# Kernel tuning notes

Measured on AMD Instinct MI355X. Metric: run time of the kernel, lower is better.

## Reference

```python
import jax, jax.numpy as jnp
import numpy as np

WS = 8          # window_size
OWS = 12        # overlap_win_size = int(8*0.5)+8
PAD = 2         # (OWS-WS)//2
HEADS = 6
DH = 16         # dim_head
INNER = HEADS * DH  # 96
SCALE = DH ** -0.5


def rel_to_abs(x):
    # x: (b, l, m) with m = 2*r - 1
    b, l, m = x.shape
    r = (m + 1) // 2
    x = jnp.concatenate([x, jnp.zeros((b, l, 1), x.dtype)], axis=2)
    flat = x.reshape(b, l * (m + 1))
    flat = jnp.concatenate([flat, jnp.zeros((b, m - l), x.dtype)], axis=1)
    final = flat.reshape(b, l + 1, m)[:, :l, m - r:]
    return final  # (b, l, r)


def relative_logits_1d(q, rel_k):
    # q: (B, X, Y, d), rel_k: (2r-1, d)
    B, X, Y, _ = q.shape
    r = (rel_k.shape[0] + 1) // 2
    logits = jnp.einsum('bxyd,rd->bxyr', q, rel_k)           # (B, X, Y, 2r-1)
    logits = rel_to_abs(logits.reshape(B * X, Y, -1)).reshape(B, X, Y, r)
    logits = jnp.broadcast_to(logits[:, :, None], (B, X, r, Y, r))  # b x i y j
    return logits


def rel_pos_emb(q, rel_height, rel_width):
    # q: (B, WS*WS, d) -> bias (B, WS*WS, OWS*OWS)
    B, _, d = q.shape
    qg = q.reshape(B, WS, WS, d)
    lw = relative_logits_1d(qg, rel_width)                   # (B, x, i, y, j)
    lw = lw.transpose(0, 1, 3, 2, 4).reshape(B, WS * WS, OWS * OWS)  # b (x y) (i j)
    lh = relative_logits_1d(qg.transpose(0, 2, 1, 3), rel_height)    # (B, y, i, x, j) roles swapped
    lh = lh.transpose(0, 3, 1, 4, 2).reshape(B, WS * WS, OWS * OWS)  # b (y x) (j i)
    return lw + lh


def unfold_windows(t, nh, nw):
    # torch nn.Unfold(kernel=OWS, stride=WS, padding=PAD) then
    # rearrange 'b (c j) i -> (b i) j c' -> (b*nh*nw, OWS*OWS, C)
    b, C, _, _ = t.shape
    tp = jnp.pad(t, ((0, 0), (0, 0), (PAD, PAD), (PAD, PAD)))
    ridx = (jnp.arange(nh) * WS)[:, None] + jnp.arange(OWS)   # (nh, OWS)
    cidx = (jnp.arange(nw) * WS)[:, None] + jnp.arange(OWS)   # (nw, OWS)
    p = tp[:, :, ridx, :]            # (b, C, nh, OWS, Wp)
    p = p[:, :, :, :, cidx]          # (b, C, nh, OWS, nw, OWS)
    p = p.transpose(0, 2, 4, 3, 5, 1)  # (b, nh, nw, OWS, OWS, C)
    return p.reshape(b * nh * nw, OWS * OWS, C)


def split_heads(t):
    # (B, n, heads*dh) -> (B*heads, n, dh)
    B, n, _ = t.shape
    return t.reshape(B, n, HEADS, DH).transpose(0, 2, 1, 3).reshape(B * HEADS, n, DH)


def setup_inputs() -> dict:
    key = jax.random.key(0)
    k = jax.random.split(key, 5)
    x = jax.random.normal(k[0], (2, 96, 256, 256), jnp.float32)
    qkv_w = jax.random.normal(k[1], (288, 96), jnp.float32) * 0.05
    qkv_b = jnp.zeros((288,), jnp.float32)
    proj_w = jax.random.normal(k[2], (96, 96), jnp.float32) * 0.05
    proj_b = jnp.zeros((96,), jnp.float32)
    rel_height = jax.random.normal(k[3], (23, 16), jnp.float32) * SCALE
    rel_width = jax.random.normal(k[4], (23, 16), jnp.float32) * SCALE
    return {"x": x, "qkv_w": qkv_w, "qkv_b": qkv_b, "proj_w": proj_w,
            "proj_b": proj_b, "rel_height": rel_height, "rel_width": rel_width}


def reference(x, qkv_w, qkv_b, proj_w, proj_b, rel_height, rel_width):
    b, c, h, w = x.shape
    nh, nw = h // WS, w // WS
    qkv = jnp.einsum('oc,bchw->bohw', qkv_w, x) + qkv_b[None, :, None, None]
    qs, ks, vs = jnp.split(qkv, 3, axis=1)  # each (b, INNER, h, w)
    # queries: non-overlapping windows 'b c (h p1) (w p2) -> (b h w) (p1 p2) c'
    qs = qs.reshape(b, INNER, nh, WS, nw, WS).transpose(0, 2, 4, 3, 5, 1)
    qs = qs.reshape(b * nh * nw, WS * WS, INNER)
    ks = unfold_windows(ks, nh, nw)  # (b*nh*nw, OWS*OWS, INNER)
    vs = unfold_windows(vs, nh, nw)
    qs, ks, vs = map(split_heads, (qs, ks, vs))  # (B*heads, n, DH)
    qs = qs * SCALE
    attn = jnp.einsum('bqd,bkd->bqk', qs, ks)
    attn = attn + rel_pos_emb(qs, rel_height, rel_width)
    attn = jax.nn.softmax(attn, axis=-1)
    out = jnp.einsum('bqk,bkd->bqd', attn, vs)  # (b*nh*nw*heads, WS*WS, DH)
    out = out.reshape(b, nh, nw, HEADS, WS, WS, DH)
    out = out.transpose(0, 3, 6, 1, 4, 2, 5).reshape(b, INNER, h, w)
    out = jnp.einsum('oc,bchw->bohw', proj_w, out) + proj_b[None, :, None, None]
    return out
```

## Files before the change

### kernel.cpp

```cpp
#include <hip/hip_runtime.h>
#include <hip/hip_bf16.h>


typedef __attribute__((ext_vector_type(8))) short bf16x8;
typedef __attribute__((ext_vector_type(4))) float f32x4;

__device__ __forceinline__ f32x4 mfma16(bf16x8 a, bf16x8 b, f32x4 c) {
  return __builtin_amdgcn_mfma_f32_16x16x32_bf16(a, b, c, 0, 0, 0);
}
__device__ __forceinline__ short f2b(float f) {
  unsigned u = __builtin_bit_cast(unsigned, f);
  unsigned r = u + 0x7fffu + ((u >> 16) & 1u);
  return (short)(r >> 16);
}
__device__ __forceinline__ unsigned cvtpk(float lo, float hi) {
  unsigned r;
  asm("v_cvt_pk_bf16_f32 %0, %1, %2" : "=v"(r) : "v"(lo), "v"(hi));
  return r;
}
__device__ __forceinline__ void splitf(float x, short& h, short& l) {
  unsigned u = __builtin_bit_cast(unsigned, x);
  h = (short)(u >> 16);
  float fh = __builtin_bit_cast(float, u & 0xffff0000u);
  l = f2b(x - fh);
}

#define KPLANE 1081600L

__global__ __launch_bounds__(256) void prep_kernel(
    const float* __restrict__ qkv_w, const float* __restrict__ proj_w,
    const float* __restrict__ rel_h, const float* __restrict__ rel_w,
    short* __restrict__ qwh, short* __restrict__ qwl,
    short* __restrict__ pwh, short* __restrict__ pwl,
    short* __restrict__ rhb, short* __restrict__ rwb,
    short* __restrict__ k_t) {
  int i = blockIdx.x * 256 + threadIdx.x;
  if (i < 288 * 96) {
    short h, l;
    splitf(qkv_w[i], h, l);
    qwh[i] = h;
    qwl[i] = l;
  }
  if (i < 96 * 96) {
    short h, l;
    splitf(proj_w[i], h, l);
    pwh[i] = h;
    pwl[i] = l;
  }
  if (i < 368) {
    rhb[i] = f2b(rel_h[i]);
    rwb[i] = f2b(rel_w[i]);
  }
  if (i < 12 * 2064) {
    int plane = i / 2064, r = i - plane * 2064;
    int py, px;
    if (r < 1040) {
      int rowid = r / 260;
      py = (rowid < 2) ? rowid : 256 + rowid;
      px = r - rowid * 260;
    } else {
      int r2 = r - 1040;
      py = 2 + (r2 >> 2);
      int cid = r2 & 3;
      px = (cid < 2) ? cid : 256 + cid;
    }
    bf16x8 z = {0, 0, 0, 0, 0, 0, 0, 0};
    long base = (long)plane * KPLANE + (long)(py * 260 + px) * 16;
    *(bf16x8*)(k_t + base) = z;
    *(bf16x8*)(k_t + base + 8) = z;
  }
}

__global__ __launch_bounds__(256) void qkv_kernel(
    const float* __restrict__ x, const short* __restrict__ qwh,
    const short* __restrict__ qwl, const float* __restrict__ bias,
    short* __restrict__ q_t, short* __restrict__ k_t,
    short* __restrict__ v_t) {
  __shared__ __attribute__((aligned(16))) short Ah[4][32][104];
  const int tid = threadIdx.x;
  const int wave = tid >> 6, lane = tid & 63;
  const int quad = lane >> 4, col = lane & 15;
  const long P0 = (long)blockIdx.x * 128 + wave * 32;
  const int b = (int)(P0 >> 16);
  const int hw0 = (int)(P0 & 65535);

  {
    const long base = ((long)b * 96) << 16;
    const int px0 = (lane & 7) * 4;
    for (int i = 0; i < 12; ++i) {
      int c = i * 8 + (lane >> 3);
      float4 v = *(const float4*)(x + base + ((long)c << 16) + hw0 + px0);
      Ah[wave][px0][c] = f2b(v.x);
      Ah[wave][px0 + 1][c] = f2b(v.y);
      Ah[wave][px0 + 2][c] = f2b(v.z);
      Ah[wave][px0 + 3][c] = f2b(v.w);
    }
  }
  bf16x8 af[2][3];
  for (int mt = 0; mt < 2; ++mt)
    for (int ks = 0; ks < 3; ++ks)
      af[mt][ks] = *(const bf16x8*)&Ah[wave][mt * 16 + col][ks * 32 + quad * 8];

  for (int t = 0; t < 3; ++t) {
    const float scale = (t == 0) ? 0.25f * 1.44269504f : 1.0f;
    for (int i6 = 0; i6 < 6; ++i6) {
      const int o = (t * 6 + i6) * 16 + col;
      bf16x8 bh[3], bl[3];
      for (int ks = 0; ks < 3; ++ks) {
        bh[ks] = *(const bf16x8*)(qwh + o * 96 + ks * 32 + quad * 8);
        bl[ks] = *(const bf16x8*)(qwl + o * 96 + ks * 32 + quad * 8);
      }
      float bv = bias[o];
      f32x4 acc0 = {bv, bv, bv, bv}, acc1 = acc0;
      for (int ks = 0; ks < 3; ++ks) {
        acc0 = mfma16(af[0][ks], bh[ks], acc0);
        acc0 = mfma16(af[0][ks], bl[ks], acc0);
        acc1 = mfma16(af[1][ks], bh[ks], acc1);
        acc1 = mfma16(af[1][ks], bl[ks], acc1);
      }
      for (int r = 0; r < 4; ++r) {
        Ah[wave][quad * 4 + r][i6 * 16 + col] = f2b(acc0[r] * scale);
        Ah[wave][16 + quad * 4 + r][i6 * 16 + col] = f2b(acc1[r] * scale);
      }
    }
    if (t == 1) {
      const int py = (hw0 >> 8) + 2;
      const int pxb = (hw0 & 255) + 2;
      for (int i = 0; i < 6; ++i) {
        int linear = i * 64 + lane;
        int px = linear / 12, c = linear - px * 12;
        int h = c >> 1, half = c & 1;
        bf16x8 vv = *(const bf16x8*)&Ah[wave][px][c * 8];
        *(bf16x8*)(k_t + (long)(h * 2 + b) * KPLANE +
                   (long)(py * 260 + pxb + px) * 16 + half * 8) = vv;
      }
    } else {
      short* plane0 = (t == 0) ? q_t : v_t;
      for (int i = 0; i < 6; ++i) {
        int linear = i * 64 + lane;
        int px = linear / 12, c = linear - px * 12;
        int h = c >> 1, half = c & 1;
        bf16x8 vv = *(const bf16x8*)&Ah[wave][px][c * 8];
        *(bf16x8*)(plane0 + (long)h * 2097152 + (P0 + px) * 16 + half * 8) =
            vv;
      }
    }
  }
}

__global__ __launch_bounds__(256) void attn_kernel(
    const short* __restrict__ q_t, const short* __restrict__ k_t,
    const short* __restrict__ v_t, const short* __restrict__ rhb,
    const short* __restrict__ rwb, short* __restrict__ ao) {
  __shared__ __attribute__((aligned(16))) short v_lds[16][168];
  __shared__ __attribute__((aligned(16))) char scratch[4][5248];

  const int orig = blockIdx.x, head = blockIdx.y;
  const int win = ((orig & 7) << 8) | (orig >> 3);
  const int b = win >> 10, wy = (win & 1023) >> 5, wx = win & 31;
  const int y0 = wy * 8 - 2, x0 = wx * 8 - 2;
  const long pb = (long)b << 16;
  const int tid = threadIdx.x;

  if (tid < 160) {
    const int key = tid;
    bool valid = false;
    long pix = 0;
    if (key < 144) {
      int kh = key / 12, kw = key - kh * 12;
      int gy = y0 + kh, gx = x0 + kw;
      valid = ((unsigned)gy < 256u) && ((unsigned)gx < 256u);
      pix = pb + gy * 256 + gx;
    }
    if (valid) {
      const short* src = v_t + (long)head * 2097152 + pix * 16;
      union { bf16x8 v; short s[8]; } u0, u1;
      u0.v = *(const bf16x8*)src;
      u1.v = *(const bf16x8*)(src + 8);
      for (int d = 0; d < 8; ++d) {
        v_lds[d][key] = u0.s[d];
        v_lds[d + 8][key] = u1.s[d];
      }
    } else {
      for (int d = 0; d < 16; ++d) v_lds[d][key] = 0;
    }
  }
  __syncthreads();

  const int wave = tid >> 6, lane = tid & 63;
  const int quad = lane >> 4, col = lane & 15;
  float* dWs = (float*)scratch[wave];
  float* dHt = dWs + 600;
  unsigned* ppd = (unsigned*)scratch[wave];

  const short* qp = q_t + (long)head * 2097152;
  const short* kpb = k_t + (long)(head * 2 + b) * KPLANE;

  bf16x8 qf = {0, 0, 0, 0, 0, 0, 0, 0};
  if (quad < 2) {
    int qg = wave * 16 + col;
    int qy = qg >> 3, qx = qg & 7;
    qf = *(const bf16x8*)(qp + (pb + (wy * 8 + qy) * 256 + wx * 8 + qx) * 16 +
                          quad * 8);
  }

  for (int nt = 0; nt < 2; ++nt) {
    int r = nt * 16 + col;
    bf16x8 bw = {0, 0, 0, 0, 0, 0, 0, 0}, bh2 = bw;
    if (quad < 2 && r < 23) {
      bw = *(const bf16x8*)(rwb + r * 16 + quad * 8);
      bh2 = *(const bf16x8*)(rhb + r * 16 + quad * 8);
    }
    f32x4 z = {0.f, 0.f, 0.f, 0.f};
    f32x4 aw = mfma16(qf, bw, z);
    f32x4 ah = mfma16(qf, bh2, z);
    if (r < 23)
      for (int r4 = 0; r4 < 4; ++r4) {
        int ql = quad * 4 + r4;
        dWs[(r + (ql & 7)) * 20 + ql] = aw[r4];
        dHt[r * 20 + ql] = ah[r4];
      }
  }

  f32x4 L[9];
  {
    int kh = (col >= 12) ? 1 : 0, kw = col - 12 * kh;
    const short* ka =
        kpb + (long)((wy * 8 + kh) * 260 + wx * 8 + kw) * 16 + quad * 8;
    for (int nt = 0; nt < 9; ++nt) {
      bf16x8 kf = *(const bf16x8*)ka;
      f32x4 z = {0.f, 0.f, 0.f, 0.f};
      L[nt] = mfma16(qf, kf, z);
      kw += 4;
      if (kw >= 12) {
        kw -= 12;
        ka += 512 * 16;
      } else {
        ka += 264 * 16;
      }
    }
  }

  const int qy4 = wave * 2 + (quad >> 1);
  {
    int kh = (col >= 12) ? 1 : 0, kw = col - 12 * kh;
    for (int nt = 0; nt < 9; ++nt) {
      f32x4 wv = *(const f32x4*)&dWs[(11 + kw) * 20 + quad * 4];
      f32x4 hv = *(const f32x4*)&dHt[(11 + kh - qy4) * 20 + quad * 4];
      for (int r4 = 0; r4 < 4; ++r4)
        L[nt][r4] = __builtin_amdgcn_exp2f(L[nt][r4] + wv[r4] + hv[r4]);
      kw += 4;
      kh += 1;
      if (kw >= 12) {
        kw -= 12;
        kh += 1;
      }
    }
  }
  asm volatile("" ::: "memory");

  for (int nt = 0; nt < 9; ++nt) {
    unsigned d0 = cvtpk(L[nt][0], L[nt][1]);
    unsigned d1 = cvtpk(L[nt][2], L[nt][3]);
    int base = (nt * 16 + col) * 9 + quad * 2;
    ppd[base] = d0;
    ppd[base + 1] = d1;
  }

  const unsigned sel = (col & 1) ? 0x07060302u : 0x05040100u;
  const bf16x8 ones = {0x3F80, 0x3F80, 0x3F80, 0x3F80,
                       0x3F80, 0x3F80, 0x3F80, 0x3F80};
  f32x4 oacc = {0.f, 0.f, 0.f, 0.f}, oaccS = oacc;
  for (int ks = 0; ks < 5; ++ks) {
    int k0 = ks * 32 + quad * 8;
    bool live = k0 < 144;
    int k0c = live ? k0 : 136;
    const unsigned* rp = ppd + k0c * 9 + (col >> 1);
    unsigned r0 = rp[0], r1 = rp[9], r2 = rp[18], r3 = rp[27];
    unsigned r4v = rp[36], r5 = rp[45], r6 = rp[54], r7 = rp[63];
    union { unsigned u[4]; bf16x8 v; } pu;
    pu.u[0] = live ? __builtin_amdgcn_perm(r1, r0, sel) : 0u;
    pu.u[1] = live ? __builtin_amdgcn_perm(r3, r2, sel) : 0u;
    pu.u[2] = live ? __builtin_amdgcn_perm(r5, r4v, sel) : 0u;
    pu.u[3] = live ? __builtin_amdgcn_perm(r7, r6, sel) : 0u;
    bf16x8 vb = *(const bf16x8*)&v_lds[col][ks * 32 + quad * 8];
    oacc = mfma16(pu.v, vb, oacc);
    oaccS = mfma16(pu.v, ones, oaccS);
  }
  for (int r4 = 0; r4 < 4; ++r4) {
    int qg = wave * 16 + quad * 4 + r4;
    int qy = qg >> 3, qx = qg & 7;
    float val = oacc[r4] * __builtin_amdgcn_rcpf(oaccS[r4]);
    ao[(long)head * 2097152 +
       (pb + (wy * 8 + qy) * 256 + wx * 8 + qx) * 16 + col] = f2b(val);
  }
}

__global__ __launch_bounds__(256) void proj_kernel(
    const short* __restrict__ ao, const short* __restrict__ pwh,
    const short* __restrict__ pwl, const float* __restrict__ bias,
    float* __restrict__ out) {
  const int tid = threadIdx.x;
  const int wave = tid >> 6, lane = tid & 63;
  const int quad = lane >> 4, col = lane & 15;
  const long P0 = (long)blockIdx.x * 128 + wave * 32;

  bf16x8 bfr[2][3];
  for (int nt = 0; nt < 2; ++nt) {
    long pix = P0 + nt * 16 + col;
    for (int ks = 0; ks < 3; ++ks) {
      int c0 = ks * 32 + quad * 8;
      bfr[nt][ks] = *(const bf16x8*)(ao + (long)(c0 >> 4) * 2097152 +
                                     pix * 16 + (c0 & 15));
    }
  }
  f32x4 acc[6][2];
  for (int mt = 0; mt < 6; ++mt) {
    for (int r = 0; r < 4; ++r) {
      float bv = bias[mt * 16 + quad * 4 + r];
      acc[mt][0][r] = bv;
      acc[mt][1][r] = bv;
    }
    bf16x8 afh[3], afl[3];
    for (int ks = 0; ks < 3; ++ks) {
      afh[ks] =
          *(const bf16x8*)(pwh + (mt * 16 + col) * 96 + ks * 32 + quad * 8);
      afl[ks] =
          *(const bf16x8*)(pwl + (mt * 16 + col) * 96 + ks * 32 + quad * 8);
    }
    for (int ks = 0; ks < 3; ++ks) {
      acc[mt][0] = mfma16(afh[ks], bfr[0][ks], acc[mt][0]);
      acc[mt][0] = mfma16(afl[ks], bfr[0][ks], acc[mt][0]);
      acc[mt][1] = mfma16(afh[ks], bfr[1][ks], acc[mt][1]);
      acc[mt][1] = mfma16(afl[ks], bfr[1][ks], acc[mt][1]);
    }
  }
  const int bb = (int)(P0 >> 16);
  const int hw0 = (int)(P0 & 65535);
  for (int mt = 0; mt < 6; ++mt)
    for (int nt = 0; nt < 2; ++nt)
      for (int r = 0; r < 4; ++r) {
        int o = mt * 16 + quad * 4 + r;
        int hw = hw0 + nt * 16 + col;
        out[(((long)(bb * 96 + o)) << 16) + hw] = acc[mt][nt][r];
      }
}

extern "C" void kernel_launch(void* const* d_in, const int* in_sizes, int n_in,
                              void* d_out, int out_size, void* d_ws,
                              size_t ws_size, hipStream_t stream) {
  const float* x = (const float*)d_in[0];
  const float* qkv_w = (const float*)d_in[1];
  const float* qkv_b = (const float*)d_in[2];
  const float* proj_w = (const float*)d_in[3];
  const float* proj_b = (const float*)d_in[4];
  const float* rel_h = (const float*)d_in[5];
  const float* rel_w = (const float*)d_in[6];

  const long NPIXC = 131072L * 96L;
  short* q_t = (short*)d_ws;
  short* k_t = q_t + NPIXC;
  short* v_t = k_t + 12 * KPLANE;
  short* ao = v_t + NPIXC;
  short* qwh = ao + NPIXC;
  short* qwl = qwh + 288 * 96;
  short* pwh = qwl + 288 * 96;
  short* pwl = pwh + 96 * 96;
  short* rhb = pwl + 96 * 96;
  short* rwb = rhb + 368;
  float* out = (float*)d_out;

  hipLaunchKernelGGL(prep_kernel, dim3(108), dim3(256), 0, stream, qkv_w,
                     proj_w, rel_h, rel_w, qwh, qwl, pwh, pwl, rhb, rwb, k_t);
  hipLaunchKernelGGL(qkv_kernel, dim3(1024), dim3(256), 0, stream, x, qwh, qwl,
                     qkv_b, q_t, k_t, v_t);
  hipLaunchKernelGGL(attn_kernel, dim3(2048, 6), dim3(256), 0, stream, q_t,
                     k_t, v_t, rhb, rwb, ao);
  hipLaunchKernelGGL(proj_kernel, dim3(1024), dim3(256), 0, stream, ao, pwh,
                     pwl, proj_b, out);
}
```

Measured before the change: 200.2 us.

## Transpose qkv and proj GEMMs so weights are the A operand and drop LDS staging

The QKV kernel now puts the weight tile in the MFMA A operand and the pixel tile in B. Input pixels load straight from global memory into registers as bf16, with no shared-memory transpose, and each wave covers 64 pixels instead of 32. The query scale is folded into the prepared weights and a precomputed scaled bias. Output columns are written as packed 32-bit stores, and the next weight slice is prefetched while the current one computes. The projection kernel gets the same restructuring, writing fp32 output in coalesced per-channel rows. The cost is more registers per thread and half as many blocks.

```diff
diff --git a/kernel.cpp b/kernel.cpp
--- a/kernel.cpp
+++ b/kernel.cpp
@@ -26,18 +26,22 @@
 }
 
 #define KPLANE 1081600L
+#define QS (0.25f * 1.44269504f)
 
 __global__ __launch_bounds__(256) void prep_kernel(
     const float* __restrict__ qkv_w, const float* __restrict__ proj_w,
     const float* __restrict__ rel_h, const float* __restrict__ rel_w,
+    const float* __restrict__ qkv_b,
     short* __restrict__ qwh, short* __restrict__ qwl,
     short* __restrict__ pwh, short* __restrict__ pwl,
     short* __restrict__ rhb, short* __restrict__ rwb,
-    short* __restrict__ k_t) {
+    float* __restrict__ sbias, short* __restrict__ k_t) {
   int i = blockIdx.x * 256 + threadIdx.x;
   if (i < 288 * 96) {
+    float wv = qkv_w[i];
+    if (i < 96 * 96) wv *= QS;
     short h, l;
-    splitf(qkv_w[i], h, l);
+    splitf(wv, h, l);
     qwh[i] = h;
     qwl[i] = l;
   }
@@ -51,6 +55,7 @@
     rhb[i] = f2b(rel_h[i]);
     rwb[i] = f2b(rel_w[i]);
   }
+  if (i < 288) sbias[i] = qkv_b[i] * (i < 96 ? QS : 1.0f);
   if (i < 12 * 2064) {
     int plane = i / 2064, r = i - plane * 2064;
     int py, px;
@@ -73,76 +78,92 @@
 
 __global__ __launch_bounds__(256) void qkv_kernel(
     const float* __restrict__ x, const short* __restrict__ qwh,
-    const short* __restrict__ qwl, const float* __restrict__ bias,
+    const short* __restrict__ qwl, const float* __restrict__ sbias,
     short* __restrict__ q_t, short* __restrict__ k_t,
     short* __restrict__ v_t) {
-  __shared__ __attribute__((aligned(16))) short Ah[4][32][104];
   const int tid = threadIdx.x;
   const int wave = tid >> 6, lane = tid & 63;
   const int quad = lane >> 4, col = lane & 15;
-  const long P0 = (long)blockIdx.x * 128 + wave * 32;
-  const int b = (int)(P0 >> 16);
-  const int hw0 = (int)(P0 & 65535);
-
-  {
-    const long base = ((long)b * 96) << 16;
-    const int px0 = (lane & 7) * 4;
-    for (int i = 0; i < 12; ++i) {
-      int c = i * 8 + (lane >> 3);
-      float4 v = *(const float4*)(x + base + ((long)c << 16) + hw0 + px0);
-      Ah[wave][px0][c] = f2b(v.x);
-      Ah[wave][px0 + 1][c] = f2b(v.y);
-      Ah[wave][px0 + 2][c] = f2b(v.z);
-      Ah[wave][px0 + 3][c] = f2b(v.w);
-    }
-  }
-  bf16x8 af[2][3];
-  for (int mt = 0; mt < 2; ++mt)
+  const int blk = blockIdx.x;
+  const int b = blk >> 8, row = blk & 255;
+
+  const float* xw = x + (((long)b * 96) << 16) + row * 256 + wave * 64 + col;
+  bf16x8 bx[4][3];
+#pragma unroll
+  for (int tile = 0; tile < 4; ++tile)
+#pragma unroll
+    for (int ks = 0; ks < 3; ++ks) {
+      const float* p = xw + tile * 16 + (((long)(ks * 32 + quad * 8)) << 16);
+      float v0 = p[0];
+      float v1 = p[1L << 16];
+      float v2 = p[2L << 16];
+      float v3 = p[3L << 16];
+      float v4 = p[4L << 16];
+      float v5 = p[5L << 16];
+      float v6 = p[6L << 16];
+      float v7 = p[7L << 16];
+      union { unsigned u[4]; bf16x8 w; } t;
+      t.u[0] = cvtpk(v0, v1);
+      t.u[1] = cvtpk(v2, v3);
+      t.u[2] = cvtpk(v4, v5);
+      t.u[3] = cvtpk(v6, v7);
+      bx[tile][ks] = t.w;
+    }
+
+  const short* wbh = qwh + col * 96 + quad * 8;
+  const short* wbl = qwl + col * 96 + quad * 8;
+  bf16x8 wh[3], wl[3];
+#pragma unroll
+  for (int ks = 0; ks < 3; ++ks) {
+    wh[ks] = *(const bf16x8*)(wbh + ks * 32);
+    wl[ks] = *(const bf16x8*)(wbl + ks * 32);
+  }
+
+  const long pixb = (long)blk * 256 + wave * 64 + col;
+  short* kbase = k_t + (long)b * KPLANE +
+                 ((long)((row + 2) * 260 + wave * 64 + col + 2)) * 16 +
+                 quad * 4;
+
+#pragma unroll
+  for (int t6 = 0; t6 < 18; ++t6) {
+    bf16x8 nh[3], nl[3];
+    if (t6 < 17) {
+#pragma unroll
+      for (int ks = 0; ks < 3; ++ks) {
+        nh[ks] = *(const bf16x8*)(wbh + (t6 + 1) * 1536 + ks * 32);
+        nl[ks] = *(const bf16x8*)(wbl + (t6 + 1) * 1536 + ks * 32);
+      }
+    }
+    f32x4 bv = *(const f32x4*)(sbias + t6 * 16 + quad * 4);
+    f32x4 acc[4] = {bv, bv, bv, bv};
+#pragma unroll
     for (int ks = 0; ks < 3; ++ks)
-      af[mt][ks] = *(const bf16x8*)&Ah[wave][mt * 16 + col][ks * 32 + quad * 8];
-
-  for (int t = 0; t < 3; ++t) {
-    const float scale = (t == 0) ? 0.25f * 1.44269504f : 1.0f;
-    for (int i6 = 0; i6 < 6; ++i6) {
-      const int o = (t * 6 + i6) * 16 + col;
-      bf16x8 bh[3], bl[3];
+#pragma unroll
+      for (int tile = 0; tile < 4; ++tile) {
+        acc[tile] = mfma16(wh[ks], bx[tile][ks], acc[tile]);
+        acc[tile] = mfma16(wl[ks], bx[tile][ks], acc[tile]);
+      }
+#pragma unroll
+    for (int tile = 0; tile < 4; ++tile) {
+      unsigned d0 = cvtpk(acc[tile][0], acc[tile][1]);
+      unsigned d1 = cvtpk(acc[tile][2], acc[tile][3]);
+      if (t6 >= 6 && t6 < 12) {
+        short* kp = kbase + (long)(t6 - 6) * (2 * KPLANE) + tile * 256;
+        *(unsigned*)kp = d0;
+        *(unsigned*)(kp + 2) = d1;
+      } else {
+        short* plane = (t6 < 6 ? q_t : v_t) +
+                       (long)(t6 < 6 ? t6 : t6 - 12) * 2097152 + pixb * 16 +
+                       tile * 256 + quad * 4;
+        *(unsigned*)plane = d0;
+        *(unsigned*)(plane + 2) = d1;
+      }
+    }
+    if (t6 < 17) {
+#pragma unroll
       for (int ks = 0; ks < 3; ++ks) {
-        bh[ks] = *(const bf16x8*)(qwh + o * 96 + ks * 32 + quad * 8);
-        bl[ks] = *(const bf16x8*)(qwl + o * 96 + ks * 32 + quad * 8);
-      }
-      float bv = bias[o];
-      f32x4 acc0 = {bv, bv, bv, bv}, acc1 = acc0;
-      for (int ks = 0; ks < 3; ++ks) {
-        acc0 = mfma16(af[0][ks], bh[ks], acc0);
-        acc0 = mfma16(af[0][ks], bl[ks], acc0);
-        acc1 = mfma16(af[1][ks], bh[ks], acc1);
-        acc1 = mfma16(af[1][ks], bl[ks], acc1);
-      }
-      for (int r = 0; r < 4; ++r) {
-        Ah[wave][quad * 4 + r][i6 * 16 + col] = f2b(acc0[r] * scale);
-        Ah[wave][16 + quad * 4 + r][i6 * 16 + col] = f2b(acc1[r] * scale);
-      }
-    }
-    if (t == 1) {
-      const int py = (hw0 >> 8) + 2;
-      const int pxb = (hw0 & 255) + 2;
-      for (int i = 0; i < 6; ++i) {
-        int linear = i * 64 + lane;
-        int px = linear / 12, c = linear - px * 12;
-        int h = c >> 1, half = c & 1;
-        bf16x8 vv = *(const bf16x8*)&Ah[wave][px][c * 8];
-        *(bf16x8*)(k_t + (long)(h * 2 + b) * KPLANE +
-                   (long)(py * 260 + pxb + px) * 16 + half * 8) = vv;
-      }
-    } else {
-      short* plane0 = (t == 0) ? q_t : v_t;
-      for (int i = 0; i < 6; ++i) {
-        int linear = i * 64 + lane;
-        int px = linear / 12, c = linear - px * 12;
-        int h = c >> 1, half = c & 1;
-        bf16x8 vv = *(const bf16x8*)&Ah[wave][px][c * 8];
-        *(bf16x8*)(plane0 + (long)h * 2097152 + (P0 + px) * 16 + half * 8) =
-            vv;
+        wh[ks] = nh[ks];
+        wl[ks] = nl[ks];
       }
     }
   }
@@ -303,47 +324,64 @@
   const int tid = threadIdx.x;
   const int wave = tid >> 6, lane = tid & 63;
   const int quad = lane >> 4, col = lane & 15;
-  const long P0 = (long)blockIdx.x * 128 + wave * 32;
-
-  bf16x8 bfr[2][3];
-  for (int nt = 0; nt < 2; ++nt) {
-    long pix = P0 + nt * 16 + col;
+  const int blk = blockIdx.x;
+  const int b = blk >> 8;
+  const long pix0 = (long)blk * 256 + wave * 64 + col;
+
+  bf16x8 bfr[4][3];
+#pragma unroll
+  for (int tile = 0; tile < 4; ++tile)
+#pragma unroll
     for (int ks = 0; ks < 3; ++ks) {
-      int c0 = ks * 32 + quad * 8;
-      bfr[nt][ks] = *(const bf16x8*)(ao + (long)(c0 >> 4) * 2097152 +
-                                     pix * 16 + (c0 & 15));
-    }
-  }
-  f32x4 acc[6][2];
+      int head = 2 * ks + (quad >> 1);
+      bfr[tile][ks] =
+          *(const bf16x8*)(ao + (long)head * 2097152 +
+                           (pix0 + tile * 16) * 16 + (quad & 1) * 8);
+    }
+
+  const short* wbh = pwh + col * 96 + quad * 8;
+  const short* wbl = pwl + col * 96 + quad * 8;
+  bf16x8 ah[3], al[3];
+#pragma unroll
+  for (int ks = 0; ks < 3; ++ks) {
+    ah[ks] = *(const bf16x8*)(wbh + ks * 32);
+    al[ks] = *(const bf16x8*)(wbl + ks * 32);
+  }
+  float* ob = out + (((long)(b * 96 + quad * 4)) << 16) + (blk & 255) * 256 +
+              wave * 64 + col;
+#pragma unroll
   for (int mt = 0; mt < 6; ++mt) {
-    for (int r = 0; r < 4; ++r) {
-      float bv = bias[mt * 16 + quad * 4 + r];
-      acc[mt][0][r] = bv;
-      acc[mt][1][r] = bv;
-    }
-    bf16x8 afh[3], afl[3];
-    for (int ks = 0; ks < 3; ++ks) {
-      afh[ks] =
-          *(const bf16x8*)(pwh + (mt * 16 + col) * 96 + ks * 32 + quad * 8);
-      afl[ks] =
-          *(const bf16x8*)(pwl + (mt * 16 + col) * 96 + ks * 32 + quad * 8);
-    }
-    for (int ks = 0; ks < 3; ++ks) {
-      acc[mt][0] = mfma16(afh[ks], bfr[0][ks], acc[mt][0]);
-      acc[mt][0] = mfma16(afl[ks], bfr[0][ks], acc[mt][0]);
-      acc[mt][1] = mfma16(afh[ks], bfr[1][ks], acc[mt][1]);
-      acc[mt][1] = mfma16(afl[ks], bfr[1][ks], acc[mt][1]);
-    }
-  }
-  const int bb = (int)(P0 >> 16);
-  const int hw0 = (int)(P0 & 65535);
-  for (int mt = 0; mt < 6; ++mt)
-    for (int nt = 0; nt < 2; ++nt)
-      for (int r = 0; r < 4; ++r) {
-        int o = mt * 16 + quad * 4 + r;
-        int hw = hw0 + nt * 16 + col;
-        out[(((long)(bb * 96 + o)) << 16) + hw] = acc[mt][nt][r];
-      }
+    bf16x8 nh[3], nl[3];
+    if (mt < 5) {
+#pragma unroll
+      for (int ks = 0; ks < 3; ++ks) {
+        nh[ks] = *(const bf16x8*)(wbh + (mt + 1) * 1536 + ks * 32);
+        nl[ks] = *(const bf16x8*)(wbl + (mt + 1) * 1536 + ks * 32);
+      }
+    }
+    f32x4 bv = *(const f32x4*)(bias + mt * 16 + quad * 4);
+    f32x4 acc[4] = {bv, bv, bv, bv};
+#pragma unroll
+    for (int ks = 0; ks < 3; ++ks)
+#pragma unroll
+      for (int tile = 0; tile < 4; ++tile) {
+        acc[tile] = mfma16(ah[ks], bfr[tile][ks], acc[tile]);
+        acc[tile] = mfma16(al[ks], bfr[tile][ks], acc[tile]);
+      }
+    float* obm = ob + ((long)(mt * 16) << 16);
+#pragma unroll
+    for (int tile = 0; tile < 4; ++tile)
+#pragma unroll
+      for (int r = 0; r < 4; ++r)
+        obm[((long)r << 16) + tile * 16] = acc[tile][r];
+    if (mt < 5) {
+#pragma unroll
+      for (int ks = 0; ks < 3; ++ks) {
+        ah[ks] = nh[ks];
+        al[ks] = nl[ks];
+      }
+    }
+  }
 }
 
 extern "C" void kernel_launch(void* const* d_in, const int* in_sizes, int n_in,
@@ -368,14 +406,16 @@
   short* pwl = pwh + 96 * 96;
   short* rhb = pwl + 96 * 96;
   short* rwb = rhb + 368;
+  float* sbias = (float*)(rwb + 368);
   float* out = (float*)d_out;
 
   hipLaunchKernelGGL(prep_kernel, dim3(108), dim3(256), 0, stream, qkv_w,
-                     proj_w, rel_h, rel_w, qwh, qwl, pwh, pwl, rhb, rwb, k_t);
-  hipLaunchKernelGGL(qkv_kernel, dim3(1024), dim3(256), 0, stream, x, qwh, qwl,
-                     qkv_b, q_t, k_t, v_t);
+                     proj_w, rel_h, rel_w, qkv_b, qwh, qwl, pwh, pwl, rhb, rwb,
+                     sbias, k_t);
+  hipLaunchKernelGGL(qkv_kernel, dim3(512), dim3(256), 0, stream, x, qwh, qwl,
+                     sbias, q_t, k_t, v_t);
   hipLaunchKernelGGL(attn_kernel, dim3(2048, 6), dim3(256), 0, stream, q_t,
                      k_t, v_t, rhb, rwb, ao);
-  hipLaunchKernelGGL(proj_kernel, dim3(1024), dim3(256), 0, stream, ao, pwh,
+  hipLaunchKernelGGL(proj_kernel, dim3(512), dim3(256), 0, stream, ao, pwh,
                      pwl, proj_b, out);
 }
```

New measurement: 195.8 us. -2.2%, faster.
